# Optimization experiments

Hardware: AMD Instinct MI355X
Metric: run time of the kernel (lower is better)

The kernel has to match this reference:

```python
import jax, jax.numpy as jnp
import numpy as np

B, S, E, H = 2, 2048, 1024, 16
HD = E // H            # head_dim = 64
ROT = 64               # rotary_dim == head_dim
BASE = 10000.0


def setup_inputs() -> dict:
    key = jax.random.key(0)
    k1, k2, k3, k4, k5 = jax.random.split(key, 5)
    return {
        "x": jax.random.normal(k1, (B, S, E), dtype=jnp.float32),
        "mask": jnp.ones((B, S), dtype=jnp.int32),
        "qkv_w": jax.random.normal(k2, (3 * E, E), dtype=jnp.float32) * (1.0 / np.sqrt(E)),
        "qkv_b": jax.random.normal(k3, (3 * E,), dtype=jnp.float32) * 0.02,
        "out_w": jax.random.normal(k4, (E, E), dtype=jnp.float32) * (1.0 / np.sqrt(E)),
        "out_b": jax.random.normal(k5, (E,), dtype=jnp.float32) * 0.02,
    }


def _rotate_half(x):
    # split last dim into (even, odd) pairs and rotate 90 degrees
    x = x.reshape(*x.shape[:-1], -1, 2)
    x1, x2 = x[..., 0], x[..., 1]
    return jnp.stack((-x2, x1), axis=-1).reshape(*x.shape[:-2], -1)


def _rope_cos_sin(seq_len, rot_dim, dtype):
    inv_freq = 1.0 / (BASE ** (jnp.arange(0, rot_dim, 2, dtype=jnp.float32) / rot_dim))
    freqs = jnp.arange(seq_len, dtype=jnp.float32)[:, None] * inv_freq[None, :]  # [S, rot/2]
    cos = jnp.repeat(jnp.cos(freqs), 2, axis=-1).astype(dtype)  # [S, rot]
    sin = jnp.repeat(jnp.sin(freqs), 2, axis=-1).astype(dtype)
    return cos, sin


def reference(x, mask, qkv_w, qkv_b, out_w, out_b):
    b, s, _ = x.shape
    qkv = x @ qkv_w.T + qkv_b                      # [B,S,3E]
    q, k, v = jnp.split(qkv, 3, axis=-1)
    shape = lambda t: t.reshape(b, s, H, HD).transpose(0, 2, 1, 3)  # [B,H,S,HD]
    q, k, v = shape(q), shape(k), shape(v)

    cos, sin = _rope_cos_sin(s, ROT, q.dtype)      # [S, ROT]
    cos = cos[None, None]                          # [1,1,S,ROT]
    sin = sin[None, None]
    q_rot, q_pass = q[..., :ROT], q[..., ROT:]
    k_rot, k_pass = k[..., :ROT], k[..., ROT:]
    q = jnp.concatenate((q_rot * cos + _rotate_half(q_rot) * sin, q_pass), axis=-1)
    k = jnp.concatenate((k_rot * cos + _rotate_half(k_rot) * sin, k_pass), axis=-1)

    scale = 1.0 / np.sqrt(HD)
    scores = jnp.einsum("bhqd,bhkd->bhqk", q, k) * scale  # [B,H,S,S]
    keep = (mask != 0)[:, None, None, :]           # [B,1,1,S]
    scores = jnp.where(keep, scores, -jnp.inf)
    attn = jax.nn.softmax(scores, axis=-1)
    context = jnp.einsum("bhqk,bhkd->bhqd", attn, v)
    context = context.transpose(0, 2, 1, 3).reshape(b, s, E)
    return context @ out_w.T + out_b
```

## Files before the change

kernel.cpp:

```cpp
#include <hip/hip_runtime.h>
#include <hip/hip_bf16.h>
#include <cmath>

#define SB 2048
#define EB 1024
#define NH 16
#define HD 64
#define KLOG 0.14391156831212788f
#define QSC 0.18033688011112042f

typedef unsigned short u16;
typedef unsigned int u32;
typedef __attribute__((ext_vector_type(8))) short short8;
typedef __attribute__((ext_vector_type(4))) float f32x4;

__device__ __forceinline__ u16 f2b(float x) {
  __hip_bfloat16 h = __float2bfloat16(x);
  return *reinterpret_cast<u16*>(&h);
}

__device__ __forceinline__ float b2f(u16 v) {
  u32 x = (u32)v << 16;
  float f;
  __builtin_memcpy(&f, &x, 4);
  return f;
}

__device__ __forceinline__ u32 pkb(float lo, float hi) {
#if __has_builtin(__builtin_amdgcn_cvt_pk_bf16_f32)
  auto v = __builtin_amdgcn_cvt_pk_bf16_f32(lo, hi);
  u32 r;
  __builtin_memcpy(&r, &v, 4);
  return r;
#else
  return (u32)f2b(lo) | ((u32)f2b(hi) << 16);
#endif
}

__device__ __forceinline__ void gl_lds16(const u16* g, u16* l) {
  __builtin_amdgcn_global_load_lds(
      (const __attribute__((address_space(1))) unsigned int*)g,
      (__attribute__((address_space(3))) unsigned int*)l, 16, 0, 0);
}

#define CN1 (4096 * 1024 / 4)
#define CN2 (3072 * 1024 / 4)
#define CN3 (1024 * 1024 / 4)
#define CNS (CN1 + CN2 + CN3)
__global__ __launch_bounds__(256) void conv_all(
    const float* __restrict__ x, const float* __restrict__ w1,
    const float* __restrict__ w2, const int* __restrict__ mask,
    u16* __restrict__ xb, u16* __restrict__ wqb, u16* __restrict__ owb,
    float* __restrict__ ctab, float* __restrict__ stab,
    float* __restrict__ fbias) {
  int i = blockIdx.x * 256 + threadIdx.x;
  if (i < CNS) {
    const float* src;
    u16* dst;
    int j;
    if (i < CN1) { src = x; dst = xb; j = i; }
    else if (i < CN1 + CN2) { src = w1; dst = wqb; j = i - CN1; }
    else { src = w2; dst = owb; j = i - CN1 - CN2; }
    float4 v = ((const float4*)src)[j];
    ushort4 o;
    o.x = f2b(v.x); o.y = f2b(v.y); o.z = f2b(v.z); o.w = f2b(v.w);
    ((ushort4*)dst)[j] = o;
  } else {
    int j = i - CNS;
    if (j < SB * 32) {
      int pos = j >> 5, p = j & 31;
      float th = (float)pos * expf(-(float)(2 * p) * KLOG);
      float sn, cs;
      sincosf(th, &sn, &cs);
      ctab[j] = cs; stab[j] = sn;
    } else {
      int j2 = j - SB * 32;
      if (j2 < 2 * SB) fbias[j2] = mask[j2] ? 0.f : -1e9f;
    }
  }
}

__global__ __launch_bounds__(256, 4) void qkv_mfma_rope(
    const u16* __restrict__ A, const u16* __restrict__ Bw,
    const float* __restrict__ bias, const float* __restrict__ ctab,
    const float* __restrict__ stab, u16* __restrict__ qb,
    u16* __restrict__ kb, u16* __restrict__ vt) {
  __shared__ u16 As[128 * 32];
  __shared__ u16 Bs[128 * 32];

  const int t = threadIdx.x;
  const int lane = t & 63, wv = t >> 6;
  const int l15 = lane & 15, quad = lane >> 4;
  const int wm = wv >> 1, wn = wv & 1;
  const int m0 = blockIdx.x * 128;
  const int n0 = blockIdx.y * 128;

  f32x4 acc[4][4] = {};

  for (int k0 = 0; k0 < 1024; k0 += 32) {
#pragma unroll
    for (int c = 0; c < 2; c++) {
      int r = wv * 32 + c * 16;
      const u16* ga = A + (size_t)(m0 + r + (lane >> 2)) * 1024 + k0 + (lane & 3) * 8;
      const u16* gb = Bw + (size_t)(n0 + r + (lane >> 2)) * 1024 + k0 + (lane & 3) * 8;
      gl_lds16(ga, &As[r * 32]);
      gl_lds16(gb, &Bs[r * 32]);
    }
    __syncthreads();

    short8 a[4], b[4];
#pragma unroll
    for (int mi = 0; mi < 4; mi++)
      a[mi] = *(const short8*)&As[(wm * 64 + mi * 16 + l15) * 32 + quad * 8];
#pragma unroll
    for (int ni = 0; ni < 4; ni++)
      b[ni] = *(const short8*)&Bs[(wn * 64 + ni * 16 + l15) * 32 + quad * 8];
#pragma unroll
    for (int mi = 0; mi < 4; mi++)
#pragma unroll
      for (int ni = 0; ni < 4; ni++)
        acc[mi][ni] = __builtin_amdgcn_mfma_f32_16x16x32_bf16(a[mi], b[ni], acc[mi][ni], 0, 0, 0);
    __syncthreads();
  }

  const int n_base = n0 + wn * 64;
  const int which = n_base >> 10;
  float b4[4];
#pragma unroll
  for (int ni = 0; ni < 4; ni++) b4[ni] = bias[n_base + ni * 16 + l15];

  const int h = (n_base & 1023) >> 6;
  const int bb = m0 >> 11;
  if (which < 2) {
    u16* dst = (which == 0) ? qb : kb;
#pragma unroll
    for (int mi = 0; mi < 4; mi++) {
#pragma unroll
      for (int r = 0; r < 4; r++) {
        int row = wm * 64 + mi * 16 + quad * 4 + r;
        int s = (m0 & 2047) + row;
        size_t obase = ((size_t)(bb * NH + h) * SB + s) * HD;
        const float* cp = ctab + (size_t)s * 32;
        const float* sp = stab + (size_t)s * 32;
#pragma unroll
        for (int ni = 0; ni < 4; ni++) {
          float v = acc[mi][ni][r] + b4[ni];
          int d = ni * 16 + l15;
          float pv = __shfl_xor(v, 1, 64);
          float c = cp[d >> 1];
          float sn_ = sp[d >> 1];
          v = v * c + pv * ((d & 1) ? sn_ : -sn_);
          if (which == 0) v *= QSC;
          dst[obase + d] = f2b(v);
        }
      }
    }
  } else {
    size_t tbase = (size_t)(bb * NH + h) * HD;
#pragma unroll
    for (int mi = 0; mi < 4; mi++) {
      int s0 = (m0 & 2047) + wm * 64 + mi * 16 + quad * 4;
#pragma unroll
      for (int ni = 0; ni < 4; ni++) {
        int d = ni * 16 + l15;
        u32 p0 = pkb(acc[mi][ni][0] + b4[ni], acc[mi][ni][1] + b4[ni]);
        u32 p1 = pkb(acc[mi][ni][2] + b4[ni], acc[mi][ni][3] + b4[ni]);
        uint2 pk = make_uint2(p0, p1);
        *(uint2*)&vt[(tbase + d) * SB + s0] = pk;
      }
    }
  }
}

__global__ __launch_bounds__(512, 4) void attn_mfma(
    const u16* __restrict__ qb, const u16* __restrict__ kb,
    const u16* __restrict__ vt, const float* __restrict__ fbias,
    u16* __restrict__ po0, u16* __restrict__ po1, float* __restrict__ pl) {
  __shared__ u16 Ks[2][4096];
  __shared__ u16 Vt[2][4096];
  __shared__ u32 Ps2[8][16][34];

  const int bh = blockIdx.x, b = bh >> 4;
  const int q0 = blockIdx.y * 256;
  const int kz = blockIdx.z;
  const int t = threadIdx.x;
  const int lane = t & 63, wv = t >> 6;
  const int l15 = lane & 15, quad = lane >> 4;

  short8 bq[2][2];
#pragma unroll
  for (int qh = 0; qh < 2; qh++) {
    const u16* qp = qb + ((size_t)bh * SB + q0 + wv * 32 + qh * 16 + l15) * HD;
    bq[qh][0] = *(const short8*)&qp[quad * 8];
    bq[qh][1] = *(const short8*)&qp[32 + quad * 8];
  }

  const u16* kbase = kb + (size_t)bh * SB * HD + (size_t)kz * 1024 * HD;
  const u16* vbase = vt + (size_t)bh * HD * SB + kz * 1024;
  const float* fbase = fbias + b * SB + kz * 1024;

  const int srow = lane >> 3;
  const int schunk = ((lane & 7) ^ srow) * 8;
  const int fslot = quad ^ (l15 & 7);

  gl_lds16(kbase + (size_t)(wv * 8 + srow) * HD + schunk, &Ks[0][wv * 512]);
  gl_lds16(vbase + (size_t)(wv * 8 + srow) * SB + schunk, &Vt[0][wv * 512]);

  f32x4 o[2][4] = {};
  float l_i[2] = {0.f, 0.f};

  for (int kt = 0; kt < 16; kt++) {
    const int bufi = kt & 1;
    __syncthreads();

    if (kt + 1 < 16) {
      size_t ko = (size_t)(kt + 1) * 64;
      gl_lds16(kbase + (ko + wv * 8 + srow) * HD + schunk, &Ks[1 - bufi][wv * 512]);
      gl_lds16(vbase + (size_t)(wv * 8 + srow) * SB + ko + schunk, &Vt[1 - bufi][wv * 512]);
    }

    f32x4 s0[4], s1[4];
#pragma unroll
    for (int mb = 0; mb < 4; mb++) {
      const u16* kr = &Ks[bufi][(mb * 16 + l15) * 64];
      short8 a0 = *(const short8*)&kr[fslot * 8];
      short8 a1 = *(const short8*)&kr[(fslot ^ 4) * 8];
      f32x4 z0 = {}, z1 = {};
      z0 = __builtin_amdgcn_mfma_f32_16x16x32_bf16(a0, bq[0][0], z0, 0, 0, 0);
      s0[mb] = __builtin_amdgcn_mfma_f32_16x16x32_bf16(a1, bq[0][1], z0, 0, 0, 0);
      z1 = __builtin_amdgcn_mfma_f32_16x16x32_bf16(a0, bq[1][0], z1, 0, 0, 0);
      s1[mb] = __builtin_amdgcn_mfma_f32_16x16x32_bf16(a1, bq[1][1], z1, 0, 0, 0);
    }

#pragma unroll
    for (int mb = 0; mb < 4; mb++) {
      f32x4 bias4 = *(const f32x4*)&fbase[kt * 64 + mb * 16 + quad * 4];
#pragma unroll
      for (int r = 0; r < 4; r++) {
        float p0 = __builtin_amdgcn_exp2f(s0[mb][r] + bias4[r]);
        float p1 = __builtin_amdgcn_exp2f(s1[mb][r] + bias4[r]);
        s0[mb][r] = p0; l_i[0] += p0;
        s1[mb][r] = p1; l_i[1] += p1;
      }
    }

    short8 pb0[2], pb1[2];
#pragma unroll
    for (int mb = 0; mb < 4; mb++) {
      uint2 w2 = make_uint2(pkb(s0[mb][0], s0[mb][1]), pkb(s0[mb][2], s0[mb][3]));
      *(uint2*)&Ps2[wv][l15][8 * mb + 2 * quad] = w2;
    }
#pragma unroll
    for (int kk = 0; kk < 2; kk++)
      pb0[kk] = *(const short8*)&Ps2[wv][l15][kk * 16 + 4 * quad];
#pragma unroll
    for (int mb = 0; mb < 4; mb++) {
      uint2 w2 = make_uint2(pkb(s1[mb][0], s1[mb][1]), pkb(s1[mb][2], s1[mb][3]));
      *(uint2*)&Ps2[wv][l15][8 * mb + 2 * quad] = w2;
    }
#pragma unroll
    for (int kk = 0; kk < 2; kk++)
      pb1[kk] = *(const short8*)&Ps2[wv][l15][kk * 16 + 4 * quad];

#pragma unroll
    for (int nb = 0; nb < 4; nb++) {
      const u16* vr = &Vt[bufi][(nb * 16 + l15) * 64];
      short8 v0 = *(const short8*)&vr[fslot * 8];
      short8 v1 = *(const short8*)&vr[(fslot ^ 4) * 8];
      o[0][nb] = __builtin_amdgcn_mfma_f32_16x16x32_bf16(v0, pb0[0], o[0][nb], 0, 0, 0);
      o[0][nb] = __builtin_amdgcn_mfma_f32_16x16x32_bf16(v1, pb0[1], o[0][nb], 0, 0, 0);
      o[1][nb] = __builtin_amdgcn_mfma_f32_16x16x32_bf16(v0, pb1[0], o[1][nb], 0, 0, 0);
      o[1][nb] = __builtin_amdgcn_mfma_f32_16x16x32_bf16(v1, pb1[1], o[1][nb], 0, 0, 0);
    }
  }

  u16* po = kz ? po1 : po0;
#pragma unroll
  for (int qh = 0; qh < 2; qh++) {
    float l = l_i[qh];
    l += __shfl_xor(l, 16, 64);
    l += __shfl_xor(l, 32, 64);
    float linv = 1.f / fmaxf(l, 1e-30f);
    int qrow = q0 + wv * 32 + qh * 16 + l15;
    size_t base = ((size_t)bh * SB + qrow) * HD;
#pragma unroll
    for (int nb = 0; nb < 4; nb++)
#pragma unroll
      for (int pr = 0; pr < 2; pr++) {
        int d = nb * 16 + quad * 4 + 2 * pr;
        *(u32*)&po[base + d] =
            pkb(o[qh][nb][2 * pr] * linv, o[qh][nb][2 * pr + 1] * linv);
      }
    if (quad == 0) pl[kz * (32 * SB) + bh * SB + qrow] = l;
  }
}

__global__ __launch_bounds__(256) void out_fused(
    const u16* __restrict__ po0, const u16* __restrict__ po1,
    const float* __restrict__ pl, const u16* __restrict__ Bw,
    const float* __restrict__ bias, float* __restrict__ out) {
  __shared__ u16 As[64 * 32];
  __shared__ u16 Bs[128 * 32];

  const int t = threadIdx.x;
  const int lane = t & 63, wv = t >> 6;
  const int l15 = lane & 15, quad = lane >> 4;
  const int wm = wv >> 1, wn = wv & 1;
  const int m0 = blockIdx.x * 64;
  const int n0 = blockIdx.y * 128;

  const int ar = t >> 2, ac = t & 3;
  const int am = m0 + ar;
  const int ab = am >> 11, aqrow = am & 2047;

  f32x4 acc[2][4] = {};

  for (int k0 = 0; k0 < 1024; k0 += 32) {
    {
      int h = k0 >> 6;
      int d = (k0 & 32) + ac * 8;
      int bh = ab * 16 + h;
      float l0 = pl[bh * SB + aqrow];
      float l1 = pl[32 * SB + bh * SB + aqrow];
      float rinv = 1.f / fmaxf(l0 + l1, 1e-30f);
      float w0 = l0 * rinv, w1 = l1 * rinv;
      size_t off = ((size_t)bh * SB + aqrow) * HD + d;
      uint4 ua = *(const uint4*)&po0[off];
      uint4 ub = *(const uint4*)&po1[off];
      const u32* pa = (const u32*)&ua;
      const u32* pq = (const u32*)&ub;
      u32 res[4];
#pragma unroll
      for (int j = 0; j < 4; j++) {
        float o0 = b2f((u16)(pa[j] & 0xffff)) * w0 + b2f((u16)(pq[j] & 0xffff)) * w1;
        float o1 = b2f((u16)(pa[j] >> 16)) * w0 + b2f((u16)(pq[j] >> 16)) * w1;
        res[j] = pkb(o0, o1);
      }
      *(uint4*)&As[ar * 32 + ac * 8] = *(const uint4*)res;
    }
#pragma unroll
    for (int c = 0; c < 2; c++) {
      int r = wv * 32 + c * 16;
      const u16* gb = Bw + (size_t)(n0 + r + (lane >> 2)) * 1024 + k0 + (lane & 3) * 8;
      gl_lds16(gb, &Bs[r * 32]);
    }
    __syncthreads();

    short8 a[2], b[4];
#pragma unroll
    for (int mi = 0; mi < 2; mi++)
      a[mi] = *(const short8*)&As[(wm * 32 + mi * 16 + l15) * 32 + quad * 8];
#pragma unroll
    for (int ni = 0; ni < 4; ni++)
      b[ni] = *(const short8*)&Bs[(wn * 64 + ni * 16 + l15) * 32 + quad * 8];
#pragma unroll
    for (int mi = 0; mi < 2; mi++)
#pragma unroll
      for (int ni = 0; ni < 4; ni++)
        acc[mi][ni] = __builtin_amdgcn_mfma_f32_16x16x32_bf16(a[mi], b[ni], acc[mi][ni], 0, 0, 0);
    __syncthreads();
  }

  float b4[4];
#pragma unroll
  for (int ni = 0; ni < 4; ni++) b4[ni] = bias[n0 + wn * 64 + ni * 16 + l15];
#pragma unroll
  for (int mi = 0; mi < 2; mi++)
#pragma unroll
    for (int r = 0; r < 4; r++) {
      int m = m0 + wm * 32 + mi * 16 + quad * 4 + r;
#pragma unroll
      for (int ni = 0; ni < 4; ni++)
        out[(size_t)m * 1024 + n0 + wn * 64 + ni * 16 + l15] = acc[mi][ni][r] + b4[ni];
    }
}

extern "C" void kernel_launch(void* const* d_in, const int* in_sizes, int n_in,
                              void* d_out, int out_size, void* d_ws, size_t ws_size,
                              hipStream_t stream) {
  const float* x     = (const float*)d_in[0];
  const int* mask    = (const int*)d_in[1];
  const float* qkv_w = (const float*)d_in[2];
  const float* qkv_b = (const float*)d_in[3];
  const float* out_w = (const float*)d_in[4];
  const float* out_b = (const float*)d_in[5];
  float* out = (float*)d_out;

  char* wsb = (char*)d_ws;
  u16* xb    = (u16*)wsb;
  u16* wqb   = (u16*)(wsb + ( 8ull << 20));
  u16* owb   = (u16*)(wsb + (14ull << 20));
  u16* qb    = (u16*)(wsb + (16ull << 20));
  u16* kb    = (u16*)(wsb + (24ull << 20));
  u16* vtb   = (u16*)(wsb + (32ull << 20));
  u16* po1   = (u16*)(wsb + (48ull << 20));
  float* ctab  = (float*)(wsb + (56ull << 20));
  float* stab  = (float*)(wsb + (56ull << 20) + (256u << 10));
  float* fbias = (float*)(wsb + (56ull << 20) + (512u << 10));
  float* pl    = (float*)(wsb + (56ull << 20) + (768u << 10));
  u16* po0   = xb;

  dim3 blk(256);
  int convBlocks = (CNS + SB * 32 + 2 * SB + 255) / 256;
  hipLaunchKernelGGL(conv_all, dim3(convBlocks), blk, 0, stream,
                     x, qkv_w, out_w, mask, xb, wqb, owb, ctab, stab, fbias);

  hipLaunchKernelGGL(qkv_mfma_rope, dim3(32, 24), blk, 0, stream,
                     xb, wqb, qkv_b, ctab, stab, qb, kb, vtb);

  hipLaunchKernelGGL(attn_mfma, dim3(32, 8, 2), dim3(512), 0, stream,
                     qb, kb, vtb, fbias, po0, po1, pl);

  hipLaunchKernelGGL(out_fused, dim3(64, 8), blk, 0, stream,
                     po0, po1, pl, owb, out_b, out);
}
```

Before: 197.2 us.

## Double-buffer LDS tiles and XOR-swizzle layout in QKV and output GEMMs

Both GEMM kernels now keep two LDS buffers and prefetch the next K-slice while MFMAs run on the current one, which also removes one barrier per iteration. In the output GEMM, the combine of the two partial attention outputs for the next slice is computed into registers ahead of time. LDS rows are XOR-swizzled on 16-byte chunks to cut bank conflicts on the fragment reads. The cost is twice the shared memory and more registers, which could reduce occupancy; out_fused also gains a launch bound of 4 blocks.

After: 202.0 us. 2.4% more time.

```diff
diff --git a/kernel.cpp b/kernel.cpp
--- a/kernel.cpp
+++ b/kernel.cpp
@@ -85,8 +85,8 @@
     const float* __restrict__ bias, const float* __restrict__ ctab,
     const float* __restrict__ stab, u16* __restrict__ qb,
     u16* __restrict__ kb, u16* __restrict__ vt) {
-  __shared__ u16 As[128 * 32];
-  __shared__ u16 Bs[128 * 32];
+  __shared__ u16 As[2][4096];
+  __shared__ u16 Bs[2][4096];
 
   const int t = threadIdx.x;
   const int lane = t & 63, wv = t >> 6;
@@ -95,33 +95,47 @@
   const int m0 = blockIdx.x * 128;
   const int n0 = blockIdx.y * 128;
 
+  const int srow = lane >> 2;
+  const int schunk = ((lane & 3) ^ (srow & 3)) * 8;
+  const u16* ga0 = A + (size_t)(m0 + wv * 32 + srow) * 1024 + schunk;
+  const u16* gb0 = Bw + (size_t)(n0 + wv * 32 + srow) * 1024 + schunk;
+  const int fslot = (quad ^ (l15 & 3)) * 8;
+
+#pragma unroll
+  for (int c = 0; c < 2; c++) {
+    gl_lds16(ga0 + c * 16 * 1024, &As[0][(wv * 32 + c * 16) * 32]);
+    gl_lds16(gb0 + c * 16 * 1024, &Bs[0][(wv * 32 + c * 16) * 32]);
+  }
+
   f32x4 acc[4][4] = {};
 
-  for (int k0 = 0; k0 < 1024; k0 += 32) {
-#pragma unroll
-    for (int c = 0; c < 2; c++) {
-      int r = wv * 32 + c * 16;
-      const u16* ga = A + (size_t)(m0 + r + (lane >> 2)) * 1024 + k0 + (lane & 3) * 8;
-      const u16* gb = Bw + (size_t)(n0 + r + (lane >> 2)) * 1024 + k0 + (lane & 3) * 8;
-      gl_lds16(ga, &As[r * 32]);
-      gl_lds16(gb, &Bs[r * 32]);
-    }
+  for (int it = 0; it < 32; it++) {
+    const int bufi = it & 1;
     __syncthreads();
 
+    if (it + 1 < 32) {
+      int k0 = (it + 1) * 32;
+#pragma unroll
+      for (int c = 0; c < 2; c++) {
+        gl_lds16(ga0 + c * 16 * 1024 + k0, &As[1 - bufi][(wv * 32 + c * 16) * 32]);
+        gl_lds16(gb0 + c * 16 * 1024 + k0, &Bs[1 - bufi][(wv * 32 + c * 16) * 32]);
+      }
+    }
+
     short8 a[4], b[4];
 #pragma unroll
     for (int mi = 0; mi < 4; mi++)
-      a[mi] = *(const short8*)&As[(wm * 64 + mi * 16 + l15) * 32 + quad * 8];
+      a[mi] = *(const short8*)&As[bufi][(wm * 64 + mi * 16 + l15) * 32 + fslot];
 #pragma unroll
     for (int ni = 0; ni < 4; ni++)
-      b[ni] = *(const short8*)&Bs[(wn * 64 + ni * 16 + l15) * 32 + quad * 8];
+      b[ni] = *(const short8*)&Bs[bufi][(wn * 64 + ni * 16 + l15) * 32 + fslot];
 #pragma unroll
     for (int mi = 0; mi < 4; mi++)
 #pragma unroll
       for (int ni = 0; ni < 4; ni++)
         acc[mi][ni] = __builtin_amdgcn_mfma_f32_16x16x32_bf16(a[mi], b[ni], acc[mi][ni], 0, 0, 0);
-    __syncthreads();
-  }
+  }
+  __syncthreads();
 
   const int n_base = n0 + wn * 64;
   const int which = n_base >> 10;
@@ -295,12 +309,12 @@
   }
 }
 
-__global__ __launch_bounds__(256) void out_fused(
+__global__ __launch_bounds__(256, 4) void out_fused(
     const u16* __restrict__ po0, const u16* __restrict__ po1,
     const float* __restrict__ pl, const u16* __restrict__ Bw,
     const float* __restrict__ bias, float* __restrict__ out) {
-  __shared__ u16 As[64 * 32];
-  __shared__ u16 Bs[128 * 32];
+  __shared__ u16 As[2][2048];
+  __shared__ u16 Bs[2][4096];
 
   const int t = threadIdx.x;
   const int lane = t & 63, wv = t >> 6;
@@ -310,55 +324,70 @@
   const int n0 = blockIdx.y * 128;
 
   const int ar = t >> 2, ac = t & 3;
+  const int aslot = ac ^ (ar & 3);
   const int am = m0 + ar;
   const int ab = am >> 11, aqrow = am & 2047;
 
+  const int srow = lane >> 2;
+  const int schunk = ((lane & 3) ^ (srow & 3)) * 8;
+  const u16* gb0 = Bw + (size_t)(n0 + wv * 32 + srow) * 1024 + schunk;
+  const int fslot = (quad ^ (l15 & 3)) * 8;
+
+  auto combineA = [&](int it, u32* res) {
+    int k0 = it * 32;
+    int h = k0 >> 6;
+    int d = (k0 & 32) + ac * 8;
+    int bh = ab * 16 + h;
+    float l0 = pl[bh * SB + aqrow];
+    float l1 = pl[32 * SB + bh * SB + aqrow];
+    float rinv = 1.f / fmaxf(l0 + l1, 1e-30f);
+    float w0 = l0 * rinv, w1 = l1 * rinv;
+    size_t off = ((size_t)bh * SB + aqrow) * HD + d;
+    uint4 ua = *(const uint4*)&po0[off];
+    uint4 ub = *(const uint4*)&po1[off];
+    const u32* pa = (const u32*)&ua;
+    const u32* pq = (const u32*)&ub;
+#pragma unroll
+    for (int j = 0; j < 4; j++) {
+      float o0 = b2f((u16)(pa[j] & 0xffff)) * w0 + b2f((u16)(pq[j] & 0xffff)) * w1;
+      float o1 = b2f((u16)(pa[j] >> 16)) * w0 + b2f((u16)(pq[j] >> 16)) * w1;
+      res[j] = pkb(o0, o1);
+    }
+  };
+
+  u32 ares[4];
+  combineA(0, ares);
+#pragma unroll
+  for (int c = 0; c < 2; c++)
+    gl_lds16(gb0 + c * 16 * 1024, &Bs[0][(wv * 32 + c * 16) * 32]);
+
   f32x4 acc[2][4] = {};
 
-  for (int k0 = 0; k0 < 1024; k0 += 32) {
-    {
-      int h = k0 >> 6;
-      int d = (k0 & 32) + ac * 8;
-      int bh = ab * 16 + h;
-      float l0 = pl[bh * SB + aqrow];
-      float l1 = pl[32 * SB + bh * SB + aqrow];
-      float rinv = 1.f / fmaxf(l0 + l1, 1e-30f);
-      float w0 = l0 * rinv, w1 = l1 * rinv;
-      size_t off = ((size_t)bh * SB + aqrow) * HD + d;
-      uint4 ua = *(const uint4*)&po0[off];
-      uint4 ub = *(const uint4*)&po1[off];
-      const u32* pa = (const u32*)&ua;
-      const u32* pq = (const u32*)&ub;
-      u32 res[4];
-#pragma unroll
-      for (int j = 0; j < 4; j++) {
-        float o0 = b2f((u16)(pa[j] & 0xffff)) * w0 + b2f((u16)(pq[j] & 0xffff)) * w1;
-        float o1 = b2f((u16)(pa[j] >> 16)) * w0 + b2f((u16)(pq[j] >> 16)) * w1;
-        res[j] = pkb(o0, o1);
-      }
-      *(uint4*)&As[ar * 32 + ac * 8] = *(const uint4*)res;
-    }
-#pragma unroll
-    for (int c = 0; c < 2; c++) {
-      int r = wv * 32 + c * 16;
-      const u16* gb = Bw + (size_t)(n0 + r + (lane >> 2)) * 1024 + k0 + (lane & 3) * 8;
-      gl_lds16(gb, &Bs[r * 32]);
-    }
+  for (int it = 0; it < 32; it++) {
+    const int bufi = it & 1;
+    *(uint4*)&As[bufi][ar * 32 + aslot * 8] = *(const uint4*)ares;
     __syncthreads();
 
+    if (it + 1 < 32) {
+      int k0 = (it + 1) * 32;
+#pragma unroll
+      for (int c = 0; c < 2; c++)
+        gl_lds16(gb0 + c * 16 * 1024 + k0, &Bs[1 - bufi][(wv * 32 + c * 16) * 32]);
+      combineA(it + 1, ares);
+    }
+
     short8 a[2], b[4];
 #pragma unroll
     for (int mi = 0; mi < 2; mi++)
-      a[mi] = *(const short8*)&As[(wm * 32 + mi * 16 + l15) * 32 + quad * 8];
+      a[mi] = *(const short8*)&As[bufi][(wm * 32 + mi * 16 + l15) * 32 + fslot];
 #pragma unroll
     for (int ni = 0; ni < 4; ni++)
-      b[ni] = *(const short8*)&Bs[(wn * 64 + ni * 16 + l15) * 32 + quad * 8];
+      b[ni] = *(const short8*)&Bs[bufi][(wn * 64 + ni * 16 + l15) * 32 + fslot];
 #pragma unroll
     for (int mi = 0; mi < 2; mi++)
 #pragma unroll
       for (int ni = 0; ni < 4; ni++)
         acc[mi][ni] = __builtin_amdgcn_mfma_f32_16x16x32_bf16(a[mi], b[ni], acc[mi][ni], 0, 0, 0);
-    __syncthreads();
   }
 
   float b4[4];
```
